# Optimization experiments

Measured on AMD Instinct MI355X. Metric: run time of the kernel, lower is better.

The kernel has to match this reference:

```python
import jax, jax.numpy as jnp
from jax import lax
import numpy as np

DN = ('NHWC', 'HWIO', 'NHWC')


def extract_patches(x, k, stride):
    # tf.image.extract_patches with sizes [1,k,k,1], strides [1,s,s,1], SAME padding.
    # Output depth ordering matches TF: (ki, kj, channel).
    B, H, W, C = x.shape
    oh = -(-H // stride)
    ow = -(-W // stride)
    ph = max((oh - 1) * stride + k - H, 0)
    pw = max((ow - 1) * stride + k - W, 0)
    xp = jnp.pad(x, ((0, 0), (ph // 2, ph - ph // 2), (pw // 2, pw - pw // 2), (0, 0)))
    cols = [xp[:, i:i + stride * (oh - 1) + 1:stride, j:j + stride * (ow - 1) + 1:stride, :]
            for i in range(k) for j in range(k)]
    return jnp.stack(cols, axis=3).reshape(B, oh, ow, k * k * C)


def contextual_attention(x, mask_s, rate=2, fuse_k=3, softmax_scale=10.0):
    B, H, W, C = x.shape
    k = rate * 2 - 1  # 3
    # raw (full-resolution) patches used as deconv filters: [B,k,k,C,L]
    raw = extract_patches(x, k, rate)
    h, w = raw.shape[1], raw.shape[2]
    L = h * w
    raw_f = raw.reshape(B, L, k, k, C).transpose(0, 2, 3, 4, 1)
    # downsample src/ref by rate (extract_patches with size 1 == strided slice)
    src = x[:, ::rate, ::rate, :]  # [B,h,w,C]
    feats = extract_patches(src, k, 1).reshape(B, L, k, k, C).transpose(0, 2, 3, 4, 1)  # [B,k,k,C,L]
    # NOTE: source normalizes by sum of squares over axes (0,1,2) = (batch,kh,kw) -> [C,L], no sqrt
    denom = jnp.maximum(jnp.sum(feats * feats, axis=(0, 1, 2)), 1e-8)
    ref_feat = feats / denom
    # mask: maxpool 16/16 then 3/1, then invert
    m = lax.reduce_window(mask_s, -jnp.inf, lax.max, (1, 16, 16, 1), (1, 16, 16, 1), 'SAME')
    m = lax.reduce_window(m, -jnp.inf, lax.max, (1, 3, 3, 1), (1, 1, 1, 1), 'SAME')
    mm = 1.0 - m  # [B,h,w,1]
    # per-sample correlation: conv src_b with its own normalized patch bank
    corr = lambda s, f: lax.conv_general_dilated(s[None], f, (1, 1), 'SAME', dimension_numbers=DN)[0]
    y = jax.vmap(corr)(src, ref_feat)  # [B,h,w,L]
    # fuse: diagonal (identity) 3x3 convs over the (query, key) score plane, both orderings
    fuse_w = jnp.eye(fuse_k, dtype=x.dtype).reshape(fuse_k, fuse_k, 1, 1)
    yi = y.reshape(B, h * w, L, 1)
    yi = lax.conv_general_dilated(yi, fuse_w, (1, 1), 'SAME', dimension_numbers=DN)
    yi = yi.reshape(B, h, w, h, w).transpose(0, 2, 1, 4, 3).reshape(B, h * w, L, 1)
    yi = lax.conv_general_dilated(yi, fuse_w, (1, 1), 'SAME', dimension_numbers=DN)
    y = yi.reshape(B, w, h, w, h).transpose(0, 2, 1, 4, 3).reshape(B, h, w, L)
    # masked softmax over reference patches
    y = jax.nn.softmax(y * mm * softmax_scale, axis=-1) * mm
    # per-sample transposed conv (paste raw patches), matching tf.nn.conv2d_transpose SAME stride=rate
    pt = max((h - 1) * rate + k - H, 0)
    pl = max((w - 1) * rate + k - W, 0)
    pad_h = (k - 1 - pt // 2, k - 1 - (pt - pt // 2))
    pad_w = (k - 1 - pl // 2, k - 1 - (pl - pl // 2))

    def deconv(y_b, f_b):
        wg = jnp.flip(f_b, axis=(0, 1)).swapaxes(2, 3)  # [k,k,L,C]
        return lax.conv_general_dilated(y_b[None], wg, (1, 1), (pad_h, pad_w),
                                        lhs_dilation=(rate, rate), dimension_numbers=DN)[0]

    y_up = jax.vmap(deconv)(y, raw_f)  # [B,H,W,C]
    return y_up, y


def gated_conv(x, w, b, dw, pw, db):
    # gen_conv_gated_ds: Conv2D -> ELU gated by SeparableConv2D -> channel softmax
    x1 = jax.nn.elu(lax.conv_general_dilated(x, w, (1, 1), 'SAME', dimension_numbers=DN) + b)
    x2 = lax.conv_general_dilated(x, dw, (1, 1), 'SAME', feature_group_count=x.shape[-1],
                                  dimension_numbers=DN)
    x2 = lax.conv_general_dilated(x2, pw, (1, 1), 'SAME', dimension_numbers=DN) + db
    return x1 * jax.nn.softmax(x2, axis=-1)


def setup_inputs():
    key = jax.random.key(0)
    ks = jax.random.split(key, 8)
    B, H, W, C, dim = 8, 64, 64, 128, 128
    s = 0.05
    x = jax.random.normal(ks[0], (B, H, W, C), jnp.float32)
    mask_s = jnp.zeros((B, 16 * H // 2, 16 * W // 2, 1), jnp.float32)
    mask_s = mask_s.at[:, 128:384, 128:384, :].set(1.0)
    return {
        'x': x,
        'mask_s': mask_s,
        'w1': jax.random.normal(ks[1], (3, 3, C, dim), jnp.float32) * s,
        'b1': jnp.zeros((dim,), jnp.float32),
        'dw1': jax.random.normal(ks[2], (3, 3, 1, C), jnp.float32) * s,
        'pw1': jax.random.normal(ks[3], (1, 1, C, dim), jnp.float32) * s,
        'db1': jnp.zeros((dim,), jnp.float32),
        'w2': jax.random.normal(ks[4], (3, 3, dim + C, dim), jnp.float32) * s,
        'b2': jnp.zeros((dim,), jnp.float32),
        'dw2': jax.random.normal(ks[5], (3, 3, 1, dim + C), jnp.float32) * s,
        'pw2': jax.random.normal(ks[6], (1, 1, dim + C, dim), jnp.float32) * s,
        'db2': jnp.zeros((dim,), jnp.float32),
    }


def reference(x, mask_s, w1, b1, dw1, pw1, db1, w2, b2, dw2, pw2, db2):
    y_up, corres = contextual_attention(x, mask_s)
    a = gated_conv(y_up, w1, b1, dw1, pw1, db1)
    a = jnp.concatenate([a, x], axis=3)
    a = gated_conv(a, w2, b2, dw2, pw2, db2)
    return a, corres
```

## Files before the change

### kernel.cpp

```cpp
#include <hip/hip_runtime.h>
#include <hip/hip_bf16.h>


#define BOFF_SP      0
#define BOFF_INVD    4734976
#define BOFF_SP16    5259264
#define BOFF_BF16    7626752
#define BOFF_T       0
#define BOFF_BP16    0
#define BOFF_YP16    18874368
#define BOFF_YUP     37748736
#define BOFF_SM      0
#define BOFF_P316    16777216
#define BOFF_A1      25698304
#define BOFF_X16     42475520
#define BOFF_WT1     69238784
#define BOFF_WT2     69828608
#define BOFF_PW1     71008256
#define BOFF_PW2     71041024
#define BOFF_M0      71106560
#define BOFF_MM      71139328

typedef float f32x4 __attribute__((ext_vector_type(4)));
typedef _Float16 f16x8 __attribute__((ext_vector_type(8)));

__global__ __launch_bounds__(256) void k_mask_pool(const float* __restrict__ mask, float* __restrict__ m0) {
    int blk = blockIdx.x;
    int b = blk >> 10, pq = blk & 1023, p = pq >> 5, q = pq & 31;
    int t = threadIdx.x, dy = t >> 4, dx = t & 15;
    float v = mask[((size_t)(b * 512 + p * 16 + dy)) * 512 + q * 16 + dx];
#pragma unroll
    for (int o = 32; o; o >>= 1) v = fmaxf(v, __shfl_xor(v, o));
    __shared__ float s[4];
    if ((t & 63) == 0) s[t >> 6] = v;
    __syncthreads();
    if (t == 0) m0[blk] = fmaxf(fmaxf(s[0], s[1]), fmaxf(s[2], s[3]));
}

__global__ void k_mask_dilate(const float* __restrict__ m0, float* __restrict__ mm) {
    int idx = blockIdx.x * 256 + threadIdx.x;
    if (idx >= 8192) return;
    int b = idx >> 10, pq = idx & 1023, p = pq >> 5, q = pq & 31;
    float v = -1e30f;
    for (int di = -1; di <= 1; ++di)
        for (int dj = -1; dj <= 1; ++dj) {
            int pp = p + di, qq = q + dj;
            if (pp >= 0 && pp < 32 && qq >= 0 && qq < 32)
                v = fmaxf(v, m0[(b << 10) + pp * 32 + qq]);
        }
    mm[idx] = 1.0f - v;
}

__global__ void k_srcpad(const float* __restrict__ x, float* __restrict__ sp) {
    int idx = blockIdx.x * 256 + threadIdx.x;
    if (idx >= 8 * 34 * 34 * 128) return;
    int c = idx & 127;
    int r = idx >> 7;
    int xx = r % 34; r /= 34;
    int yy = r % 34; int b = r / 34;
    float v = 0.f;
    if (yy >= 1 && yy <= 32 && xx >= 1 && xx <= 32)
        v = x[(((size_t)(b * 64 + (yy - 1) * 2)) * 64 + (xx - 1) * 2) * 128 + c];
    sp[idx] = v;
}

__global__ void k_sp16(const float* __restrict__ sp, _Float16* __restrict__ o) {
    int idx = blockIdx.x * 256 + threadIdx.x;
    if (idx >= 147968) return;
    const float* s = sp + (size_t)idx * 8;
    float4 v0 = *reinterpret_cast<const float4*>(s);
    float4 v1 = *reinterpret_cast<const float4*>(s + 4);
    f16x8 h;
    h[0] = (_Float16)v0.x; h[1] = (_Float16)v0.y; h[2] = (_Float16)v0.z; h[3] = (_Float16)v0.w;
    h[4] = (_Float16)v1.x; h[5] = (_Float16)v1.y; h[6] = (_Float16)v1.z; h[7] = (_Float16)v1.w;
    *reinterpret_cast<f16x8*>(o + (size_t)idx * 8) = h;
}

__global__ void k_invd(const float* __restrict__ sp, float* __restrict__ invd) {
    int idx = blockIdx.x * 256 + threadIdx.x;
    if (idx >= 1024 * 128) return;
    int c = idx & 127, l = idx >> 7, lh = l >> 5, lw = l & 31;
    float s = 0.f;
    for (int b = 0; b < 8; ++b)
#pragma unroll
        for (int i = 0; i < 3; ++i)
#pragma unroll
            for (int j = 0; j < 3; ++j) {
                float v = sp[(((size_t)(b * 34 + lh + i)) * 34 + (lw + j)) * 128 + c];
                s += v * v;
            }
    invd[idx] = 1.0f / fmaxf(s, 1e-8f);
}

__global__ void k_corr_B16(const float* __restrict__ sp, const float* __restrict__ invd,
                           _Float16* __restrict__ bf) {
    int idx = blockIdx.x * 256 + threadIdx.x;
    if (idx >= 1179648) return;
    int c8 = idx & 15; int rest = idx >> 4;
    int ij = rest % 9; int rest2 = rest / 9;
    int l = rest2 & 1023, b = rest2 >> 10;
    int lh = l >> 5, lw = l & 31;
    int i = (ij >= 6) ? 2 : (ij >= 3 ? 1 : 0);
    int j = ij - 3 * i;
    int c0 = c8 * 8;
    const float* s = sp + (((size_t)(b * 34 + lh + i)) * 34 + (lw + j)) * 128 + c0;
    const float* dv = invd + l * 128 + c0;
    f16x8 h;
#pragma unroll
    for (int u = 0; u < 8; ++u) h[u] = (_Float16)(s[u] * dv[u]);
    size_t off = ((size_t)(b * 1024 + l)) * 1152 + ij * 128 + c0;
    *reinterpret_cast<f16x8*>(bf + off) = h;
}

__global__ void k_deconv_B16(const float* __restrict__ x, _Float16* __restrict__ bp) {
    int idx = blockIdx.x * 256 + threadIdx.x;
    if (idx >= 1179648) return;
    int l8 = idx & 127; int rest = idx >> 7;
    int c = rest & 127; int rest2 = rest >> 7;
    int ij = rest2 % 9; int b = rest2 / 9;
    int ip = (ij >= 6) ? 2 : (ij >= 3 ? 1 : 0);
    int jp = ij - 3 * ip;
    int l0 = l8 * 8;
    int lh = l0 >> 5, lw0 = l0 & 31;
    int rr = 2 * lh + ip;
    f16x8 h;
#pragma unroll
    for (int u = 0; u < 8; ++u) {
        int ss = 2 * (lw0 + u) + jp;
        float v = (rr < 64 && ss < 64) ? x[(((size_t)(b * 64 + rr)) * 64 + ss) * 128 + c] : 0.f;
        h[u] = (_Float16)v;
    }
    size_t off = (((size_t)(b * 9 + ij)) * 128 + c) * 1024 + l0;
    *reinterpret_cast<f16x8*>(bp + off) = h;
}

__global__ __launch_bounds__(512) void k_corr_mfma(const _Float16* __restrict__ sp16,
                                                   const _Float16* __restrict__ bf,
                                                   float* __restrict__ outy) {
    const int b = blockIdx.z, tm = blockIdx.y, tn = blockIdx.x;
    __shared__ _Float16 A16[128][40];
    const int tid = threadIdx.x;
    const int w = tid >> 6, lane = tid & 63, m = lane & 15, g = lane >> 4;
    const int rh = w & 1, cg = w >> 1;
    f32x4 acc[4];
#pragma unroll
    for (int mf = 0; mf < 4; ++mf) acc[mf] = f32x4{0.f, 0.f, 0.f, 0.f};
    const int srow = tid >> 2, scc = (tid & 3) * 8;
    const int pq = tm * 128 + srow, p = pq >> 5, q = pq & 31;
    const int col0 = tn * 64 + cg * 16 + m;
    const size_t boff = ((size_t)b * 1024 + col0) * 1152 + g * 8;

    auto aoff = [&](int kt) -> size_t {
        int ij = kt >> 7;
        int i = (ij >= 6) ? 2 : (ij >= 3 ? 1 : 0);
        int j = ij - 3 * i;
        int c0 = (kt & 127) + scc;
        return (((size_t)(b * 34 + p + i)) * 34 + (q + j)) * 128 + c0;
    };
    f16x8 ar = *reinterpret_cast<const f16x8*>(sp16 + aoff(0));
    f16x8 nb = *reinterpret_cast<const f16x8*>(bf + boff);

    for (int kt = 0; kt < 1152; kt += 32) {
        __syncthreads();
        *reinterpret_cast<f16x8*>(&A16[srow][scc]) = ar;
        __syncthreads();
        const int ktn = (kt + 32 < 1152) ? kt + 32 : kt;
        f16x8 cb = nb;
        ar = *reinterpret_cast<const f16x8*>(sp16 + aoff(ktn));
        nb = *reinterpret_cast<const f16x8*>(bf + boff + ktn);

        f16x8 av[4];
#pragma unroll
        for (int mf = 0; mf < 4; ++mf)
            av[mf] = *reinterpret_cast<const f16x8*>(&A16[rh * 64 + mf * 16 + m][g * 8]);
#pragma unroll
        for (int mf = 0; mf < 4; ++mf)
            acc[mf] = __builtin_amdgcn_mfma_f32_16x16x32_f16(av[mf], cb, acc[mf], 0, 0, 0);
    }
#pragma unroll
    for (int mf = 0; mf < 4; ++mf) {
        int row = tm * 128 + rh * 64 + mf * 16 + g * 4;
#pragma unroll
        for (int r = 0; r < 4; ++r)
            outy[((size_t)b << 20) + (size_t)(row + r) * 1024 + col0] = acc[mf][r];
    }
}

__global__ __launch_bounds__(512) void k_deconv_mfma(const _Float16* __restrict__ yp16,
                                                     const _Float16* __restrict__ bp,
                                                     float* __restrict__ yup) {
    const int b = blockIdx.z, tm = blockIdx.y, tn = blockIdx.x;
    __shared__ _Float16 A16[128][40];
    const int tid = threadIdx.x;
    const int w = tid >> 6, lane = tid & 63, m = lane & 15, g = lane >> 4;
    const int rh = w & 1, cg = w >> 1;
    f32x4 acc[4][2];
#pragma unroll
    for (int mf = 0; mf < 4; ++mf)
#pragma unroll
        for (int nn = 0; nn < 2; ++nn) acc[mf][nn] = f32x4{0.f, 0.f, 0.f, 0.f};
    const int srow = tid >> 2, scc = (tid & 3) * 8;
    const int c0 = cg * 32 + m;
    const _Float16* abase = yp16 + ((size_t)b << 20) + (size_t)(tm * 128 + srow) * 1024 + scc;
    const size_t boff0 = (((size_t)(b * 9 + tn)) * 128 + c0) * 1024 + g * 8;
    const size_t boff1 = (((size_t)(b * 9 + tn)) * 128 + c0 + 16) * 1024 + g * 8;

    f16x8 ar = *reinterpret_cast<const f16x8*>(abase);
    f16x8 nb0 = *reinterpret_cast<const f16x8*>(bp + boff0);
    f16x8 nb1 = *reinterpret_cast<const f16x8*>(bp + boff1);

    for (int kt = 0; kt < 1024; kt += 32) {
        __syncthreads();
        *reinterpret_cast<f16x8*>(&A16[srow][scc]) = ar;
        __syncthreads();
        const int ktn = (kt + 32 < 1024) ? kt + 32 : kt;
        f16x8 cb0 = nb0, cb1 = nb1;
        ar = *reinterpret_cast<const f16x8*>(abase + ktn);
        nb0 = *reinterpret_cast<const f16x8*>(bp + boff0 + ktn);
        nb1 = *reinterpret_cast<const f16x8*>(bp + boff1 + ktn);

        f16x8 av[4];
#pragma unroll
        for (int mf = 0; mf < 4; ++mf)
            av[mf] = *reinterpret_cast<const f16x8*>(&A16[rh * 64 + mf * 16 + m][g * 8]);
#pragma unroll
        for (int mf = 0; mf < 4; ++mf) {
            acc[mf][0] = __builtin_amdgcn_mfma_f32_16x16x32_f16(av[mf], cb0, acc[mf][0], 0, 0, 0);
            acc[mf][1] = __builtin_amdgcn_mfma_f32_16x16x32_f16(av[mf], cb1, acc[mf][1], 0, 0, 0);
        }
    }
    const int ip = (tn >= 6) ? 2 : (tn >= 3 ? 1 : 0);
    const int jp = tn - 3 * ip;
#pragma unroll
    for (int mf = 0; mf < 4; ++mf) {
        int uvb = tm * 128 + rh * 64 + mf * 16 + g * 4;
#pragma unroll
        for (int nn = 0; nn < 2; ++nn) {
            int c = c0 + nn * 16;
#pragma unroll
            for (int r = 0; r < 4; ++r) {
                int uv = uvb + r;
                int uu = uv >> 5, vv = uv & 31;
                int P = 2 * uu + ip, Q = 2 * vv + jp;
                if (P < 64 && Q < 64)
                    atomicAdd(&yup[(((size_t)(b * 64 + P)) * 64 + Q) * 128 + c], acc[mf][nn][r]);
            }
        }
    }
}

__global__ void k_fuse1(const float* __restrict__ in, float* __restrict__ out) {
    size_t idx = (size_t)blockIdx.x * 256 + threadIdx.x;
    if (idx >= (size_t)8 * 1024 * 1024) return;
    int t = (int)(idx & 1023);
    int s = (int)((idx >> 10) & 1023);
    int b = (int)(idx >> 20);
    const float* base = in + ((size_t)b << 20);
    float v = base[(size_t)s * 1024 + t];
    if (s > 0 && t > 0) v += base[(size_t)(s - 1) * 1024 + (t - 1)];
    if (s < 1023 && t < 1023) v += base[(size_t)(s + 1) * 1024 + (t + 1)];
    out[idx] = v;
}

__global__ void k_fuse2(const float* __restrict__ in, float* __restrict__ out) {
    size_t idx = (size_t)blockIdx.x * 256 + threadIdx.x;
    if (idx >= (size_t)8 * 1024 * 1024) return;
    int t = (int)(idx & 1023);
    int s = (int)((idx >> 10) & 1023);
    int b = (int)(idx >> 20);
    int m0 = ((s & 31) << 5) + (s >> 5);
    int n0 = ((t & 31) << 5) + (t >> 5);
    const float* base = in + ((size_t)b << 20);
    float v = 0.f;
#pragma unroll
    for (int d = -1; d <= 1; ++d) {
        int m = m0 + d, n = n0 + d;
        if (m >= 0 && m < 1024 && n >= 0 && n < 1024)
            v += base[(size_t)(((m & 31) << 5) + (m >> 5)) * 1024 + (((n & 31) << 5) + (n >> 5))];
    }
    out[idx] = v;
}

__global__ __launch_bounds__(256) void k_softmax1024(const float* __restrict__ yv,
                                                     const float* __restrict__ mm,
                                                     float* __restrict__ outc,
                                                     _Float16* __restrict__ yp16) {
    int row = blockIdx.x;
    const float* base = yv + (size_t)row * 1024;
    float mmv = mm[row];
    int t = threadIdx.x;
    float vals[4];
    float mx = -1e30f;
#pragma unroll
    for (int i = 0; i < 4; ++i) {
        vals[i] = base[t + i * 256] * mmv * 10.0f;
        mx = fmaxf(mx, vals[i]);
    }
#pragma unroll
    for (int o = 32; o; o >>= 1) mx = fmaxf(mx, __shfl_xor(mx, o));
    __shared__ float red[8];
    if ((t & 63) == 0) red[t >> 6] = mx;
    __syncthreads();
    mx = fmaxf(fmaxf(red[0], red[1]), fmaxf(red[2], red[3]));
    float s = 0.f;
#pragma unroll
    for (int i = 0; i < 4; ++i) {
        vals[i] = expf(vals[i] - mx);
        s += vals[i];
    }
#pragma unroll
    for (int o = 32; o; o >>= 1) s += __shfl_xor(s, o);
    if ((t & 63) == 0) red[4 + (t >> 6)] = s;
    __syncthreads();
    s = red[4] + red[5] + red[6] + red[7];
    float inv = mmv / s;
#pragma unroll
    for (int i = 0; i < 4; ++i) {
        float pv = vals[i] * inv;
        outc[(size_t)row * 1024 + t + i * 256] = pv;
        yp16[(size_t)row * 1024 + t + i * 256] = (_Float16)pv;
    }
}

__global__ __launch_bounds__(256) void k_pad16(const float* __restrict__ in,
                                               _Float16* __restrict__ o) {
    int idx = blockIdx.x * 256 + threadIdx.x;
    int c8 = idx & 15;
    int r = idx >> 4;
    int pc = r % 66; r /= 66;
    int pr = r % 66; int b = r / 66;
    f16x8 h;
    if (pr >= 1 && pr <= 64 && pc >= 1 && pc <= 64) {
        const float* s = in + (((size_t)(b * 64 + pr - 1)) * 64 + (pc - 1)) * 128 + c8 * 8;
        float4 v0 = *reinterpret_cast<const float4*>(s);
        float4 v1 = *reinterpret_cast<const float4*>(s + 4);
        h[0] = (_Float16)v0.x; h[1] = (_Float16)v0.y; h[2] = (_Float16)v0.z; h[3] = (_Float16)v0.w;
        h[4] = (_Float16)v1.x; h[5] = (_Float16)v1.y; h[6] = (_Float16)v1.z; h[7] = (_Float16)v1.w;
    } else {
#pragma unroll
        for (int u = 0; u < 8; ++u) h[u] = (_Float16)0.f;
    }
    *reinterpret_cast<f16x8*>(o + (size_t)idx * 8) = h;
}

__global__ void k_wt16(const float* __restrict__ w, _Float16* __restrict__ o, int CI) {
    int idx = blockIdx.x * 256 + threadIdx.x;
    if (idx >= 9 * CI * 128) return;
    int ci = idx % CI; int rest = idx / CI;
    int co = rest & 127; int ij = rest >> 7;
    o[idx] = (_Float16)w[((size_t)ij * CI + ci) * 128 + co];
}

__global__ void k_pw16(const float* __restrict__ pw, _Float16* __restrict__ out, int CI) {
    int idx = blockIdx.x * 256 + threadIdx.x;
    if (idx >= CI * 128) return;
    int co = idx & 127, ci = idx >> 7;
    out[(size_t)co * CI + ci] = (_Float16)pw[idx];
}

template <int CI>
__global__ __launch_bounds__(256, 2) void k_dwpw_mfma(const _Float16* __restrict__ in0,
                                                      const _Float16* __restrict__ in1,
                                                      const float* __restrict__ dwW,
                                                      const _Float16* __restrict__ pwt,
                                                      const float* __restrict__ db,
                                                      float* __restrict__ smout) {
    const int bid = blockIdx.x;
    const int swz = (bid & 7) * 64 + (bid >> 3);
    const int b = swz >> 6, P = swz & 63;
    const int t = threadIdx.x;
    const int w = t >> 6, lane = t & 63, m = lane & 15, g = lane >> 4;
    __shared__ _Float16 Adw[64 * CI];
    __shared__ float red[2][4][64];
    char* ab = (char*)Adw;
    const int px = lane;
    const int cb = w * (CI / 4);
    float dwacc[CI / 4];
#pragma unroll
    for (int u = 0; u < CI / 4; ++u) dwacc[u] = 0.f;
#pragma unroll
    for (int i = 0; i < 3; ++i) {
#pragma unroll
        for (int j = 0; j < 3; ++j) {
            const int ij = i * 3 + j;
#pragma unroll
            for (int c8 = 0; c8 < CI / 32; ++c8) {
                const int c = cb + c8 * 8;
                const _Float16* ph = (CI == 256 && c >= 128) ? in1 : in0;
                const int cc = (CI == 256 && c >= 128) ? (c - 128) : c;
                size_t off = (((size_t)b * 66 + P + i) * 66 + px + j) * 128 + cc;
                f16x8 vh = *reinterpret_cast<const f16x8*>(ph + off);
#pragma unroll
                for (int u = 0; u < 8; ++u)
                    dwacc[c8 * 8 + u] = fmaf((float)vh[u], dwW[ij * CI + c + u], dwacc[c8 * 8 + u]);
            }
        }
    }
#pragma unroll
    for (int c8 = 0; c8 < CI / 32; ++c8) {
        f16x8 hv;
#pragma unroll
        for (int u = 0; u < 8; ++u) hv[u] = (_Float16)dwacc[c8 * 8 + u];
        int byte = px * (CI * 2) + (cb + c8 * 8) * 2;
        int sz = byte ^ ((px & 7) << 4);
        *reinterpret_cast<f16x8*>(ab + sz) = hv;
    }
    __syncthreads();
    f32x4 acc[4][2];
#pragma unroll
    for (int mt = 0; mt < 4; ++mt)
#pragma unroll
        for (int nn = 0; nn < 2; ++nn) acc[mt][nn] = f32x4{0.f, 0.f, 0.f, 0.f};
    const int co0 = w * 32 + m;
#pragma unroll
    for (int kc = 0; kc < CI / 32; ++kc) {
        f16x8 av[4];
#pragma unroll
        for (int mt = 0; mt < 4; ++mt) {
            int prow = mt * 16 + m;
            int byte = prow * (CI * 2) + (kc * 32 + g * 8) * 2;
            int sz = byte ^ ((prow & 7) << 4);
            av[mt] = *reinterpret_cast<const f16x8*>(ab + sz);
        }
#pragma unroll
        for (int nn = 0; nn < 2; ++nn) {
            f16x8 bv = *reinterpret_cast<const f16x8*>(pwt + (size_t)(co0 + nn * 16) * CI + kc * 32 + g * 8);
#pragma unroll
            for (int mt = 0; mt < 4; ++mt)
                acc[mt][nn] = __builtin_amdgcn_mfma_f32_16x16x32_f16(av[mt], bv, acc[mt][nn], 0, 0, 0);
        }
    }
    float db0 = db[co0], db1 = db[co0 + 16];
    float mx[4][4];
#pragma unroll
    for (int mt = 0; mt < 4; ++mt)
#pragma unroll
        for (int r = 0; r < 4; ++r) {
            acc[mt][0][r] += db0;
            acc[mt][1][r] += db1;
            float v = fmaxf(acc[mt][0][r], acc[mt][1][r]);
#pragma unroll
            for (int o = 1; o <= 8; o <<= 1) v = fmaxf(v, __shfl_xor(v, o));
            mx[mt][r] = v;
        }
    if (m == 0) {
#pragma unroll
        for (int mt = 0; mt < 4; ++mt)
#pragma unroll
            for (int r = 0; r < 4; ++r) red[0][w][mt * 16 + g * 4 + r] = mx[mt][r];
    }
    __syncthreads();
    float sume[4][4];
#pragma unroll
    for (int mt = 0; mt < 4; ++mt)
#pragma unroll
        for (int r = 0; r < 4; ++r) {
            int p = mt * 16 + g * 4 + r;
            float M = fmaxf(fmaxf(red[0][0][p], red[0][1][p]), fmaxf(red[0][2][p], red[0][3][p]));
            acc[mt][0][r] = expf(acc[mt][0][r] - M);
            acc[mt][1][r] = expf(acc[mt][1][r] - M);
            float s = acc[mt][0][r] + acc[mt][1][r];
#pragma unroll
            for (int o = 1; o <= 8; o <<= 1) s += __shfl_xor(s, o);
            sume[mt][r] = s;
        }
    if (m == 0) {
#pragma unroll
        for (int mt = 0; mt < 4; ++mt)
#pragma unroll
            for (int r = 0; r < 4; ++r) red[1][w][mt * 16 + g * 4 + r] = sume[mt][r];
    }
    __syncthreads();
#pragma unroll
    for (int mt = 0; mt < 4; ++mt)
#pragma unroll
        for (int r = 0; r < 4; ++r) {
            int p = mt * 16 + g * 4 + r;
            float S = red[1][0][p] + red[1][1][p] + red[1][2][p] + red[1][3][p];
            float inv = 1.0f / S;
            size_t pix = ((size_t)b * 64 + P) * 64 + p;
            smout[pix * 128 + co0] = acc[mt][0][r] * inv;
            smout[pix * 128 + co0 + 16] = acc[mt][1][r] * inv;
        }
}

template <int CI>
__global__ __launch_bounds__(256, 4) void k_conv_lds(const _Float16* __restrict__ in0,
                                                     const _Float16* __restrict__ in1,
                                                     const _Float16* __restrict__ wt,
                                                     const float* __restrict__ bias,
                                                     const float* __restrict__ sm,
                                                     float* __restrict__ out) {
    const int bid = blockIdx.x;
    const int idx = (bid & 7) * 128 + (bid >> 3);
    const int row = idx >> 1, cohalf = idx & 1;
    const int b = row >> 6, P = row & 63;
    const int tid = threadIdx.x;
    const int w = tid >> 6, lane = tid & 63;
    const int m = lane & 15, g = lane >> 4;
    __shared__ _Float16 S[66 * 128];
    char* sb = (char*)S;
    f32x4 acc[4];
#pragma unroll
    for (int mt = 0; mt < 4; ++mt) acc[mt] = f32x4{0.f, 0.f, 0.f, 0.f};
    const int cow = cohalf * 64 + w * 16 + m;

#pragma unroll
    for (int half = 0; half < CI / 128; ++half) {
        const _Float16* ih = (half == 0) ? in0 : in1;
        const size_t rbase0 = ((size_t)b * 66 + P) * 66 * 128;
#pragma unroll
        for (int i = 0; i < 3; ++i) {
            __syncthreads();
            const size_t rsrc = rbase0 + (size_t)i * 66 * 128;
#pragma unroll
            for (int e0 = 0; e0 < 1056; e0 += 256) {
                int e = e0 + tid;
                if (e < 1056) {
                    int px = e >> 4, c8 = e & 15;
                    int lin = px * 256 + c8 * 16;
                    int sz = lin ^ ((px & 7) << 4);
                    size_t so = rsrc + (size_t)px * 128 + c8 * 8;
                    *reinterpret_cast<f16x8*>(sb + sz) = *reinterpret_cast<const f16x8*>(ih + so);
                }
            }
            __syncthreads();
#pragma unroll
            for (int j = 0; j < 3; ++j) {
                const int ij = i * 3 + j;
                const _Float16* wp = wt + ((size_t)ij * 128 + cow) * CI + half * 128 + g * 8;
#pragma unroll
                for (int ci0 = 0; ci0 < 128; ci0 += 32) {
                    f16x8 bv = *reinterpret_cast<const f16x8*>(wp + ci0);
                    f16x8 av[4];
#pragma unroll
                    for (int mt = 0; mt < 4; ++mt) {
                        int px = mt * 16 + m + j;
                        int lin = px * 256 + ci0 * 2 + g * 16;
                        int sz = lin ^ ((px & 7) << 4);
                        av[mt] = *reinterpret_cast<const f16x8*>(sb + sz);
                    }
#pragma unroll
                    for (int mt = 0; mt < 4; ++mt)
                        acc[mt] = __builtin_amdgcn_mfma_f32_16x16x32_f16(av[mt], bv, acc[mt], 0, 0, 0);
                }
            }
        }
    }
    const float bb = bias[cow];
#pragma unroll
    for (int mt = 0; mt < 4; ++mt) {
#pragma unroll
        for (int r = 0; r < 4; ++r) {
            int Q = mt * 16 + g * 4 + r;
            size_t pix = ((size_t)b * 64 + P) * 64 + Q;
            float z = acc[mt][r] + bb;
            z = z > 0.f ? z : expm1f(z);
            out[pix * 128 + cow] = z * sm[pix * 128 + cow];
        }
    }
}

extern "C" void kernel_launch(void* const* d_in, const int* in_sizes, int n_in,
                              void* d_out, int out_size, void* d_ws, size_t ws_size,
                              hipStream_t stream) {
    const float* x    = (const float*)d_in[0];
    const float* mask = (const float*)d_in[1];
    const float* w1   = (const float*)d_in[2];
    const float* b1   = (const float*)d_in[3];
    const float* dw1  = (const float*)d_in[4];
    const float* pw1  = (const float*)d_in[5];
    const float* db1  = (const float*)d_in[6];
    const float* w2   = (const float*)d_in[7];
    const float* b2   = (const float*)d_in[8];
    const float* dw2  = (const float*)d_in[9];
    const float* pw2  = (const float*)d_in[10];
    const float* db2  = (const float*)d_in[11];

    float* out_a = (float*)d_out;
    float* out_c = out_a + 4194304;

    char* wsb = (char*)d_ws;
    float* sp      = (float*)(wsb + BOFF_SP);
    float* invd    = (float*)(wsb + BOFF_INVD);
    _Float16* sp16 = (_Float16*)(wsb + BOFF_SP16);
    _Float16* bf16b = (_Float16*)(wsb + BOFF_BF16);
    float* Tbuf    = (float*)(wsb + BOFF_T);
    _Float16* bp16 = (_Float16*)(wsb + BOFF_BP16);
    _Float16* yp16 = (_Float16*)(wsb + BOFF_YP16);
    float* yup     = (float*)(wsb + BOFF_YUP);
    float* smb     = (float*)(wsb + BOFF_SM);
    _Float16* p316 = (_Float16*)(wsb + BOFF_P316);
    float* a1      = (float*)(wsb + BOFF_A1);
    _Float16* x16  = (_Float16*)(wsb + BOFF_X16);
    _Float16* wt1  = (_Float16*)(wsb + BOFF_WT1);
    _Float16* wt2  = (_Float16*)(wsb + BOFF_WT2);
    _Float16* pw1t = (_Float16*)(wsb + BOFF_PW1);
    _Float16* pw2t = (_Float16*)(wsb + BOFF_PW2);
    float* m0      = (float*)(wsb + BOFF_M0);
    float* mmb     = (float*)(wsb + BOFF_MM);

    k_mask_pool<<<8192, 256, 0, stream>>>(mask, m0);
    k_mask_dilate<<<32, 256, 0, stream>>>(m0, mmb);
    k_srcpad<<<4624, 256, 0, stream>>>(x, sp);
    k_sp16<<<579, 256, 0, stream>>>(sp, sp16);
    k_invd<<<512, 256, 0, stream>>>(sp, invd);
    k_wt16<<<576, 256, 0, stream>>>(w1, wt1, 128);
    k_wt16<<<1152, 256, 0, stream>>>(w2, wt2, 256);
    k_pw16<<<64, 256, 0, stream>>>(pw1, pw1t, 128);
    k_pw16<<<128, 256, 0, stream>>>(pw2, pw2t, 256);
    k_corr_B16<<<4608, 256, 0, stream>>>(sp, invd, bf16b);
    k_corr_mfma<<<dim3(16, 8, 8), 512, 0, stream>>>(sp16, bf16b, out_c);
    k_fuse1<<<32768, 256, 0, stream>>>(out_c, Tbuf);
    k_fuse2<<<32768, 256, 0, stream>>>(Tbuf, out_c);
    k_deconv_B16<<<4608, 256, 0, stream>>>(x, bp16);
    k_softmax1024<<<8192, 256, 0, stream>>>(out_c, mmb, out_c, yp16);
    hipMemsetAsync(yup, 0, (size_t)4194304 * sizeof(float), stream);
    k_deconv_mfma<<<dim3(9, 8, 8), 512, 0, stream>>>(yp16, bp16, yup);
    k_pad16<<<2178, 256, 0, stream>>>(yup, p316);
    k_pad16<<<2178, 256, 0, stream>>>(x, x16);
    k_dwpw_mfma<128><<<512, 256, 0, stream>>>(p316, nullptr, dw1, pw1t, db1, smb);
    k_conv_lds<128><<<1024, 256, 0, stream>>>(p316, nullptr, wt1, b1, smb, a1);
    k_pad16<<<2178, 256, 0, stream>>>(a1, p316);
    k_dwpw_mfma<256><<<512, 256, 0, stream>>>(p316, x16, dw2, pw2t, db2, smb);
    k_conv_lds<256><<<1024, 256, 0, stream>>>(p316, x16, wt2, b2, smb, out_a);
}
```

Before: 434.5 us.

## Drop LDS staging in MFMA GEMMs and remap blocks for XCD-aware L2 reuse

The correlation and deconvolution MFMA kernels now load their A fragments straight from global memory into registers, one per M-fragment, with a one-step register prefetch. This removes the LDS staging and both __syncthreads per K step. The 3D grid is flattened to 1D, and block IDs are remapped so the blocks sharing a B panel (same batch and column tile) are placed on the same XCD, which should improve L2 reuse. The cost is four times more global A loads per thread, since A rows are no longer shared across waves through LDS, plus more registers per thread.

```diff
diff --git a/kernel.cpp b/kernel.cpp
--- a/kernel.cpp
+++ b/kernel.cpp
@@ -137,45 +137,47 @@
 __global__ __launch_bounds__(512) void k_corr_mfma(const _Float16* __restrict__ sp16,
                                                    const _Float16* __restrict__ bf,
                                                    float* __restrict__ outy) {
-    const int b = blockIdx.z, tm = blockIdx.y, tn = blockIdx.x;
-    __shared__ _Float16 A16[128][40];
+    const int bid = blockIdx.x;
+    const int xcd = bid & 7, slot = bid >> 3;
+    const int tm = slot & 7, pg = slot >> 3;
+    const int panel = pg * 8 + xcd;
+    const int b = panel >> 4, tn = panel & 15;
     const int tid = threadIdx.x;
     const int w = tid >> 6, lane = tid & 63, m = lane & 15, g = lane >> 4;
     const int rh = w & 1, cg = w >> 1;
     f32x4 acc[4];
 #pragma unroll
     for (int mf = 0; mf < 4; ++mf) acc[mf] = f32x4{0.f, 0.f, 0.f, 0.f};
-    const int srow = tid >> 2, scc = (tid & 3) * 8;
-    const int pq = tm * 128 + srow, p = pq >> 5, q = pq & 31;
     const int col0 = tn * 64 + cg * 16 + m;
     const size_t boff = ((size_t)b * 1024 + col0) * 1152 + g * 8;
-
-    auto aoff = [&](int kt) -> size_t {
+    int pA[4], qA[4];
+#pragma unroll
+    for (int mf = 0; mf < 4; ++mf) {
+        int pq = tm * 128 + rh * 64 + mf * 16 + m;
+        pA[mf] = pq >> 5; qA[mf] = pq & 31;
+    }
+    auto aoff = [&](int kt, int mf) -> size_t {
         int ij = kt >> 7;
         int i = (ij >= 6) ? 2 : (ij >= 3 ? 1 : 0);
         int j = ij - 3 * i;
-        int c0 = (kt & 127) + scc;
-        return (((size_t)(b * 34 + p + i)) * 34 + (q + j)) * 128 + c0;
+        return (((size_t)(b * 34 + pA[mf] + i)) * 34 + (qA[mf] + j)) * 128 + (kt & 127) + g * 8;
     };
-    f16x8 ar = *reinterpret_cast<const f16x8*>(sp16 + aoff(0));
-    f16x8 nb = *reinterpret_cast<const f16x8*>(bf + boff);
+    f16x8 na[4], nb;
+#pragma unroll
+    for (int mf = 0; mf < 4; ++mf) na[mf] = *reinterpret_cast<const f16x8*>(sp16 + aoff(0, mf));
+    nb = *reinterpret_cast<const f16x8*>(bf + boff);
 
     for (int kt = 0; kt < 1152; kt += 32) {
-        __syncthreads();
-        *reinterpret_cast<f16x8*>(&A16[srow][scc]) = ar;
-        __syncthreads();
         const int ktn = (kt + 32 < 1152) ? kt + 32 : kt;
-        f16x8 cb = nb;
-        ar = *reinterpret_cast<const f16x8*>(sp16 + aoff(ktn));
+        f16x8 ca[4], cb = nb;
+#pragma unroll
+        for (int mf = 0; mf < 4; ++mf) ca[mf] = na[mf];
+#pragma unroll
+        for (int mf = 0; mf < 4; ++mf) na[mf] = *reinterpret_cast<const f16x8*>(sp16 + aoff(ktn, mf));
         nb = *reinterpret_cast<const f16x8*>(bf + boff + ktn);
-
-        f16x8 av[4];
 #pragma unroll
         for (int mf = 0; mf < 4; ++mf)
-            av[mf] = *reinterpret_cast<const f16x8*>(&A16[rh * 64 + mf * 16 + m][g * 8]);
-#pragma unroll
-        for (int mf = 0; mf < 4; ++mf)
-            acc[mf] = __builtin_amdgcn_mfma_f32_16x16x32_f16(av[mf], cb, acc[mf], 0, 0, 0);
+            acc[mf] = __builtin_amdgcn_mfma_f32_16x16x32_f16(ca[mf], cb, acc[mf], 0, 0, 0);
     }
 #pragma unroll
     for (int mf = 0; mf < 4; ++mf) {
@@ -189,8 +191,11 @@
 __global__ __launch_bounds__(512) void k_deconv_mfma(const _Float16* __restrict__ yp16,
                                                      const _Float16* __restrict__ bp,
                                                      float* __restrict__ yup) {
-    const int b = blockIdx.z, tm = blockIdx.y, tn = blockIdx.x;
-    __shared__ _Float16 A16[128][40];
+    const int bid = blockIdx.x;
+    const int xcd = bid & 7, slot = bid >> 3;
+    const int tm = slot & 7, pg = slot >> 3;
+    const int panel = pg * 8 + xcd;
+    const int b = panel / 9, tn = panel % 9;
     const int tid = threadIdx.x;
     const int w = tid >> 6, lane = tid & 63, m = lane & 15, g = lane >> 4;
     const int rh = w & 1, cg = w >> 1;
@@ -199,34 +204,34 @@
     for (int mf = 0; mf < 4; ++mf)
 #pragma unroll
         for (int nn = 0; nn < 2; ++nn) acc[mf][nn] = f32x4{0.f, 0.f, 0.f, 0.f};
-    const int srow = tid >> 2, scc = (tid & 3) * 8;
     const int c0 = cg * 32 + m;
-    const _Float16* abase = yp16 + ((size_t)b << 20) + (size_t)(tm * 128 + srow) * 1024 + scc;
     const size_t boff0 = (((size_t)(b * 9 + tn)) * 128 + c0) * 1024 + g * 8;
     const size_t boff1 = (((size_t)(b * 9 + tn)) * 128 + c0 + 16) * 1024 + g * 8;
-
-    f16x8 ar = *reinterpret_cast<const f16x8*>(abase);
-    f16x8 nb0 = *reinterpret_cast<const f16x8*>(bp + boff0);
-    f16x8 nb1 = *reinterpret_cast<const f16x8*>(bp + boff1);
+    const _Float16* arow[4];
+#pragma unroll
+    for (int mf = 0; mf < 4; ++mf) {
+        int uv = tm * 128 + rh * 64 + mf * 16 + m;
+        arow[mf] = yp16 + ((size_t)b << 20) + (size_t)uv * 1024 + g * 8;
+    }
+    f16x8 na[4], nb0, nb1;
+#pragma unroll
+    for (int mf = 0; mf < 4; ++mf) na[mf] = *reinterpret_cast<const f16x8*>(arow[mf]);
+    nb0 = *reinterpret_cast<const f16x8*>(bp + boff0);
+    nb1 = *reinterpret_cast<const f16x8*>(bp + boff1);
 
     for (int kt = 0; kt < 1024; kt += 32) {
-        __syncthreads();
-        *reinterpret_cast<f16x8*>(&A16[srow][scc]) = ar;
-        __syncthreads();
         const int ktn = (kt + 32 < 1024) ? kt + 32 : kt;
-        f16x8 cb0 = nb0, cb1 = nb1;
-        ar = *reinterpret_cast<const f16x8*>(abase + ktn);
+        f16x8 ca[4], cb0 = nb0, cb1 = nb1;
+#pragma unroll
+        for (int mf = 0; mf < 4; ++mf) ca[mf] = na[mf];
+#pragma unroll
+        for (int mf = 0; mf < 4; ++mf) na[mf] = *reinterpret_cast<const f16x8*>(arow[mf] + ktn);
         nb0 = *reinterpret_cast<const f16x8*>(bp + boff0 + ktn);
         nb1 = *reinterpret_cast<const f16x8*>(bp + boff1 + ktn);
-
-        f16x8 av[4];
-#pragma unroll
-        for (int mf = 0; mf < 4; ++mf)
-            av[mf] = *reinterpret_cast<const f16x8*>(&A16[rh * 64 + mf * 16 + m][g * 8]);
 #pragma unroll
         for (int mf = 0; mf < 4; ++mf) {
-            acc[mf][0] = __builtin_amdgcn_mfma_f32_16x16x32_f16(av[mf], cb0, acc[mf][0], 0, 0, 0);
-            acc[mf][1] = __builtin_amdgcn_mfma_f32_16x16x32_f16(av[mf], cb1, acc[mf][1], 0, 0, 0);
+            acc[mf][0] = __builtin_amdgcn_mfma_f32_16x16x32_f16(ca[mf], cb0, acc[mf][0], 0, 0, 0);
+            acc[mf][1] = __builtin_amdgcn_mfma_f32_16x16x32_f16(ca[mf], cb1, acc[mf][1], 0, 0, 0);
         }
     }
     const int ip = (tn >= 6) ? 2 : (tn >= 3 ? 1 : 0);
@@ -610,13 +615,13 @@
     k_pw16<<<64, 256, 0, stream>>>(pw1, pw1t, 128);
     k_pw16<<<128, 256, 0, stream>>>(pw2, pw2t, 256);
     k_corr_B16<<<4608, 256, 0, stream>>>(sp, invd, bf16b);
-    k_corr_mfma<<<dim3(16, 8, 8), 512, 0, stream>>>(sp16, bf16b, out_c);
+    k_corr_mfma<<<1024, 512, 0, stream>>>(sp16, bf16b, out_c);
     k_fuse1<<<32768, 256, 0, stream>>>(out_c, Tbuf);
     k_fuse2<<<32768, 256, 0, stream>>>(Tbuf, out_c);
     k_deconv_B16<<<4608, 256, 0, stream>>>(x, bp16);
     k_softmax1024<<<8192, 256, 0, stream>>>(out_c, mmb, out_c, yp16);
     hipMemsetAsync(yup, 0, (size_t)4194304 * sizeof(float), stream);
-    k_deconv_mfma<<<dim3(9, 8, 8), 512, 0, stream>>>(yp16, bp16, yup);
+    k_deconv_mfma<<<576, 512, 0, stream>>>(yp16, bp16, yup);
     k_pad16<<<2178, 256, 0, stream>>>(yup, p316);
     k_pad16<<<2178, 256, 0, stream>>>(x, x16);
     k_dwpw_mfma<128><<<512, 256, 0, stream>>>(p316, nullptr, dw1, pw1t, db1, smb);
```

Measured after the change: 609.7 us. 1.4x slower.
